# Optimization experiments

Measured on AMD Instinct MI355X. Metric: run time of the kernel, lower is better.

## Reference

```python
import jax, jax.numpy as jnp
import numpy as np

B, S, D, H = 4, 1024, 1024, 16
HD = D // H  # head_dim = 64


def setup_inputs() -> dict:
    key = jax.random.key(0)
    ks = jax.random.split(key, 12)
    inp = {
        "query": jax.random.normal(ks[0], (B, S, D), jnp.float32),
        "key": jax.random.normal(ks[1], (B, S, D), jnp.float32),
        "value": jax.random.normal(ks[2], (B, S, D), jnp.float32),
        # padding mask: 0 = masked, 1 = keep; broadcastable to [B,H,Sq,Sk]
        "mask": jax.random.randint(ks[3], (B, 1, 1, S), 0, 2, jnp.int32),
        # Dense params (Glorot-ish scale)
        "Wq": jax.random.normal(ks[4], (D, D), jnp.float32) / np.sqrt(D),
        "bq": jnp.zeros((D,), jnp.float32),
        "Wk": jax.random.normal(ks[5], (D, D), jnp.float32) / np.sqrt(D),
        "bk": jnp.zeros((D,), jnp.float32),
        "Wv": jax.random.normal(ks[6], (D, D), jnp.float32) / np.sqrt(D),
        "bv": jnp.zeros((D,), jnp.float32),
        "Wo": jax.random.normal(ks[7], (D, D), jnp.float32) / np.sqrt(D),
        "bo": jnp.zeros((D,), jnp.float32),
    }
    return inp


def _split_heads(x):
    # [B, S, D] -> [B, H, S, HD]
    b, s, _ = x.shape
    return x.reshape(b, s, H, HD).transpose(0, 2, 1, 3)


def reference(query, key, value, mask, Wq, bq, Wk, bk, Wv, bv, Wo, bo):
    q = _split_heads(query @ Wq + bq)   # [B,H,S,HD]
    k = _split_heads(key @ Wk + bk)
    v = _split_heads(value @ Wv + bv)

    scale = jnp.sqrt(jnp.asarray(HD, q.dtype))
    energy = jnp.einsum("bhqd,bhkd->bhqk", q, k) / scale  # [B,H,S,S]
    energy = jnp.where(mask == 0, jnp.asarray(-1e10, energy.dtype), energy)
    attention = jax.nn.softmax(energy, axis=-1)
    # dropout is identity at inference
    x = jnp.einsum("bhqk,bhkd->bhqd", attention, v)       # [B,H,S,HD]
    x = x.transpose(0, 2, 1, 3).reshape(query.shape[0], -1, H * HD)  # [B,S,D]
    outputs = x @ Wo + bo
    return outputs, attention
```

## Files before the change

kernel.cpp:

```cpp
#include <hip/hip_runtime.h>

typedef short short8  __attribute__((ext_vector_type(8)));
typedef short short4v __attribute__((ext_vector_type(4)));
typedef float float4v __attribute__((ext_vector_type(4)));
typedef int   int4v   __attribute__((ext_vector_type(4)));

__device__ __forceinline__ short f2bf(float f) {
    unsigned u = __builtin_bit_cast(unsigned, f);
    u += 0x7fff + ((u >> 16) & 1);
    return (short)(u >> 16);
}

__device__ __forceinline__ void gl_lds16(const void* g, void* l) {
    __builtin_amdgcn_global_load_lds(
        (const __attribute__((address_space(1))) void*)g,
        (__attribute__((address_space(3))) void*)l, 16, 0, 0);
}

__global__ __launch_bounds__(256) void prep(
    const float* __restrict__ W0, const float* __restrict__ W1,
    const float* __restrict__ W2, const float* __restrict__ W3,
    short* __restrict__ T0, short* __restrict__ T1,
    short* __restrict__ T2, short* __restrict__ T3,
    const float* __restrict__ qf, const float* __restrict__ kf,
    const float* __restrict__ vf,
    short* __restrict__ Qb, short* __restrict__ Kb, short* __restrict__ Vb)
{
    __shared__ short Tl[64 * 72];
    const int tid = threadIdx.x;
    if (blockIdx.x >= 1024) {
        int cid = blockIdx.x - 1024;
        int arr = cid >> 11;
        const float* src = arr == 0 ? qf : arr == 1 ? kf : vf;
        short*       dst = arr == 0 ? Qb : arr == 1 ? Kb : Vb;
        size_t base = ((size_t)(cid & 2047) * 256 + tid) * 8;
        float4v v0 = *(const float4v*)&src[base];
        float4v v1 = *(const float4v*)&src[base + 4];
        short8 o = {f2bf(v0[0]), f2bf(v0[1]), f2bf(v0[2]), f2bf(v0[3]),
                    f2bf(v1[0]), f2bf(v1[1]), f2bf(v1[2]), f2bf(v1[3])};
        *(short8*)&dst[base] = o;
        return;
    }
    const int mat = blockIdx.x >> 8;
    const int t   = blockIdx.x & 255;
    const int k0 = (t >> 4) * 64, n0 = (t & 15) * 64;
    const float* W = mat == 0 ? W0 : mat == 1 ? W1 : mat == 2 ? W2 : W3;
    short*       T = mat == 0 ? T0 : mat == 1 ? T1 : mat == 2 ? T2 : T3;
    #pragma unroll
    for (int i = 0; i < 4; i++) {
        int c = tid + i * 256;
        int row = c >> 4, c4 = (c & 15) * 4;
        float4v v = *(const float4v*)&W[(size_t)(k0 + row) * 1024 + n0 + c4];
        short4v s = {f2bf(v[0]), f2bf(v[1]), f2bf(v[2]), f2bf(v[3])};
        *(short4v*)&Tl[row * 72 + c4] = s;
    }
    __syncthreads();
    #pragma unroll
    for (int i = 0; i < 2; i++) {
        int c = tid + i * 256;
        int nrow = c >> 3, k8 = (c & 7) * 8;
        short8 v;
        #pragma unroll
        for (int e = 0; e < 8; e++) v[e] = Tl[(k8 + e) * 72 + nrow];
        *(short8*)&T[(size_t)(n0 + nrow) * 1024 + k0 + k8] = v;
    }
}

__device__ __forceinline__ void gemm_body(
    const short* __restrict__ A, const short* __restrict__ Bt,
    short* As, short* Bs, float4v (&acc)[4][2], int m0, int n0, int K)
{
    const int tid = threadIdx.x;
    const int w = tid >> 6, lid = tid & 63, quad = lid >> 4, l15 = lid & 15;
    const int wr = w >> 1, wc = w & 1;
    const int lrow = lid >> 3, lcb = lid & 7;

    for (int kb = 0; kb < K; kb += 64) {
        #pragma unroll
        for (int p = 0; p < 4; p++) {
            int chunk = p * 4 + w;
            int row = chunk * 8 + lrow;
            int cb = lcb ^ (row & 7);
            gl_lds16(&A[(size_t)(m0 + row) * K + kb + cb * 8], &As[chunk * 512]);
        }
        #pragma unroll
        for (int p = 0; p < 2; p++) {
            int chunk = p * 4 + w;
            int row = chunk * 8 + lrow;
            int cb = lcb ^ (row & 7);
            gl_lds16(&Bt[(size_t)(n0 + row) * K + kb + cb * 8], &Bs[chunk * 512]);
        }
        __syncthreads();

        short8 af[4][2], bfr[2][2];
        #pragma unroll
        for (int i = 0; i < 4; i++) {
            int row = wr * 64 + i * 16 + l15;
            int sw = row & 7;
            #pragma unroll
            for (int h = 0; h < 2; h++)
                af[i][h] = *(short8*)&As[row * 64 + ((h * 4 + quad) ^ sw) * 8];
        }
        #pragma unroll
        for (int j = 0; j < 2; j++) {
            int row = wc * 32 + j * 16 + l15;
            int sw = row & 7;
            #pragma unroll
            for (int h = 0; h < 2; h++)
                bfr[j][h] = *(short8*)&Bs[row * 64 + ((h * 4 + quad) ^ sw) * 8];
        }
        #pragma unroll
        for (int i = 0; i < 4; i++)
            #pragma unroll
            for (int j = 0; j < 2; j++) {
                acc[i][j] = __builtin_amdgcn_mfma_f32_16x16x32_bf16(
                    af[i][0], bfr[j][0], acc[i][j], 0, 0, 0);
                acc[i][j] = __builtin_amdgcn_mfma_f32_16x16x32_bf16(
                    af[i][1], bfr[j][1], acc[i][j], 0, 0, 0);
            }
        __syncthreads();
    }
}

__global__ __launch_bounds__(256) void gemm_qkv(
    const short* __restrict__ Ab, const short* __restrict__ Btb,
    const float* __restrict__ b0, const float* __restrict__ b1,
    const float* __restrict__ b2, short* __restrict__ Cq,
    short* __restrict__ Ck, short* __restrict__ Cvt)
{
    __shared__ short As[128 * 64];
    __shared__ short Bs[64 * 64];
    const int zz = blockIdx.z;
    const short* A  = Ab  + (size_t)zz * 4194304;
    const short* Bt = Btb + (size_t)zz * 1048576;
    const float* bias = zz == 0 ? b0 : zz == 1 ? b1 : b2;
    const int m0 = blockIdx.x * 128, n0 = blockIdx.y * 64;

    float4v acc[4][2];
    #pragma unroll
    for (int i = 0; i < 4; i++)
        #pragma unroll
        for (int j = 0; j < 2; j++) acc[i][j] = (float4v){0.f, 0.f, 0.f, 0.f};

    gemm_body(A, Bt, As, Bs, acc, m0, n0, 1024);

    const int tid = threadIdx.x;
    const int w = tid >> 6, lid = tid & 63, quad = lid >> 4, l15 = lid & 15;
    const int wr = w >> 1, wc = w & 1;
    #pragma unroll
    for (int j = 0; j < 2; j++) {
        int n = n0 + wc * 32 + j * 16 + l15;
        float bj = bias[n];
        #pragma unroll
        for (int i = 0; i < 4; i++) {
            if (zz == 2) {
                int b = m0 >> 10;
                int sbase = (m0 & 1023) + wr * 64 + i * 16 + quad * 4;
                short4v sv;
                #pragma unroll
                for (int r = 0; r < 4; r++) sv[r] = f2bf(acc[i][j][r] + bj);
                *(short4v*)&Cvt[(size_t)b * 1048576 + (size_t)n * 1024 + sbase] = sv;
            } else {
                short* C = zz == 0 ? Cq : Ck;
                #pragma unroll
                for (int r = 0; r < 4; r++) {
                    int m = m0 + wr * 64 + i * 16 + quad * 4 + r;
                    C[(size_t)m * 1024 + n] = f2bf(acc[i][j][r] + bj);
                }
            }
        }
    }
}

__global__ __launch_bounds__(256) void gemm_out(
    const short* __restrict__ A, const short* __restrict__ Bt,
    const float* __restrict__ bias, float* __restrict__ C)
{
    __shared__ short As[128 * 64];
    __shared__ short Bs[64 * 64];
    const int m0 = blockIdx.x * 128, n0 = blockIdx.y * 64;
    float4v acc[4][2];
    #pragma unroll
    for (int i = 0; i < 4; i++)
        #pragma unroll
        for (int j = 0; j < 2; j++) acc[i][j] = (float4v){0.f, 0.f, 0.f, 0.f};

    gemm_body(A, Bt, As, Bs, acc, m0, n0, 1024);

    const int tid = threadIdx.x;
    const int w = tid >> 6, lid = tid & 63, quad = lid >> 4, l15 = lid & 15;
    const int wr = w >> 1, wc = w & 1;
    #pragma unroll
    for (int j = 0; j < 2; j++) {
        int n = n0 + wc * 32 + j * 16 + l15;
        float bj = bias[n];
        #pragma unroll
        for (int i = 0; i < 4; i++)
            #pragma unroll
            for (int r = 0; r < 4; r++) {
                int m = m0 + wr * 64 + i * 16 + quad * 4 + r;
                C[(size_t)m * 1024 + n] = acc[i][j][r] + bj;
            }
    }
}

__global__ __launch_bounds__(256, 4) void attn_kernel(
    const short* __restrict__ Qp, const short* __restrict__ Kp,
    const short* __restrict__ Vt, const int* __restrict__ mask,
    float* __restrict__ attnOut, short* __restrict__ X)
{
    __shared__ float SH[4608];
    __shared__ int   maskl[1024];
    __shared__ float redm[4][16];
    __shared__ float redl[4][16];

    const int tid = threadIdx.x;
    const int w = tid >> 6, lid = tid & 63, quad = lid >> 4, l15 = lid & 15;
    const int bid = blockIdx.x;
    const int qb = bid & 63;
    const int bh = bid >> 6;
    const int b = bh >> 4, h = bh & 15;
    const int q0 = qb * 16;
    const size_t rowbase = (size_t)b * 1048576;
    const size_t hoff = (size_t)h * 64;

    *(int4v*)&maskl[tid * 4] = *(const int4v*)&mask[b * 1024 + tid * 4];

    short8 aq0 = *(const short8*)
        &Qp[rowbase + (size_t)(q0 + l15) * 1024 + hoff + quad * 8];
    short8 aq1 = *(const short8*)
        &Qp[rowbase + (size_t)(q0 + l15) * 1024 + hoff + 32 + quad * 8];
    __syncthreads();

    float m_r[4] = {-3e38f, -3e38f, -3e38f, -3e38f};
    float l_r[4] = {0.f, 0.f, 0.f, 0.f};
    #pragma unroll
    for (int nk = 0; nk < 8; nk++) {
        #pragma unroll
        for (int jj = 0; jj < 2; jj++) {
            int n = nk * 128 + w * 32 + jj * 16 + l15;
            const short* kr = &Kp[rowbase + (size_t)n * 1024 + hoff + quad * 8];
            short8 kf0 = *(const short8*)kr;
            short8 kf1 = *(const short8*)(kr + 32);
            float4v acc = (float4v){0.f, 0.f, 0.f, 0.f};
            acc = __builtin_amdgcn_mfma_f32_16x16x32_bf16(aq0, kf0, acc, 0, 0, 0);
            acc = __builtin_amdgcn_mfma_f32_16x16x32_bf16(aq1, kf1, acc, 0, 0, 0);
            bool keep = maskl[n] != 0;
            #pragma unroll
            for (int r = 0; r < 4; r++) {
                float s = keep ? acc[r] * 0.125f : -1e10f;
                float mn = fmaxf(m_r[r], s);
                l_r[r] = l_r[r] * __expf(m_r[r] - mn) + __expf(s - mn);
                m_r[r] = mn;
            }
        }
    }
    #pragma unroll
    for (int off = 1; off < 16; off <<= 1) {
        #pragma unroll
        for (int r = 0; r < 4; r++) {
            float mo = __shfl_xor(m_r[r], off);
            float lo = __shfl_xor(l_r[r], off);
            float mn = fmaxf(m_r[r], mo);
            l_r[r] = l_r[r] * __expf(m_r[r] - mn) + lo * __expf(mo - mn);
            m_r[r] = mn;
        }
    }
    if (l15 == 0) {
        #pragma unroll
        for (int r = 0; r < 4; r++) {
            redm[w][quad * 4 + r] = m_r[r];
            redl[w][quad * 4 + r] = l_r[r];
        }
    }
    __syncthreads();
    float mrow[4], inv[4];
    #pragma unroll
    for (int r = 0; r < 4; r++) {
        int qr = quad * 4 + r;
        float m0 = redm[0][qr], m1 = redm[1][qr];
        float m2 = redm[2][qr], m3 = redm[3][qr];
        float M = fmaxf(fmaxf(m0, m1), fmaxf(m2, m3));
        float L = redl[0][qr] * __expf(m0 - M) + redl[1][qr] * __expf(m1 - M)
                + redl[2][qr] * __expf(m2 - M) + redl[3][qr] * __expf(m3 - M);
        mrow[r] = M;
        inv[r] = 1.0f / L;
    }

    const size_t abase = ((size_t)bh * 1024 + q0) * 1024;
    float* Pw0 = &SH[(size_t)(0 * 4 + w) * 16 * 36];
    float* Pw1 = &SH[(size_t)(1 * 4 + w) * 16 * 36];
    float4v accX[4];
    #pragma unroll
    for (int jj = 0; jj < 4; jj++) accX[jj] = (float4v){0.f, 0.f, 0.f, 0.f};

    #pragma unroll
    for (int kt = 0; kt < 8; kt++) {
        float* Pw = (kt & 1) ? Pw1 : Pw0;
        #pragma unroll
        for (int jj2 = 0; jj2 < 2; jj2++) {
            int n = kt * 128 + w * 32 + jj2 * 16 + l15;
            const short* kr = &Kp[rowbase + (size_t)n * 1024 + hoff + quad * 8];
            short8 kf0 = *(const short8*)kr;
            short8 kf1 = *(const short8*)(kr + 32);
            float4v acc = (float4v){0.f, 0.f, 0.f, 0.f};
            acc = __builtin_amdgcn_mfma_f32_16x16x32_bf16(aq0, kf0, acc, 0, 0, 0);
            acc = __builtin_amdgcn_mfma_f32_16x16x32_bf16(aq1, kf1, acc, 0, 0, 0);
            bool keep = maskl[n] != 0;
            #pragma unroll
            for (int r = 0; r < 4; r++) {
                float s = keep ? acc[r] * 0.125f : -1e10f;
                float p = __expf(s - mrow[r]) * inv[r];
                Pw[(quad * 4 + r) * 36 + jj2 * 16 + l15] = p;
            }
        }
        #pragma unroll
        for (int pass = 0; pass < 2; pass++) {
            int row = pass * 8 + (lid >> 3), c4 = (lid & 7) * 4;
            float4v pv = *(float4v*)&Pw[row * 36 + c4];
            __builtin_nontemporal_store(pv, (float4v*)
                &attnOut[abase + (size_t)row * 1024 + kt * 128 + w * 32 + c4]);
        }
        float4v pa0 = *(float4v*)&Pw[l15 * 36 + quad * 8];
        float4v pa1 = *(float4v*)&Pw[l15 * 36 + quad * 8 + 4];
        short8 ap = {f2bf(pa0[0]), f2bf(pa0[1]), f2bf(pa0[2]), f2bf(pa0[3]),
                     f2bf(pa1[0]), f2bf(pa1[1]), f2bf(pa1[2]), f2bf(pa1[3])};
        #pragma unroll
        for (int jj = 0; jj < 4; jj++) {
            short8 bv = *(const short8*)
                &Vt[rowbase + (hoff + jj * 16 + l15) * 1024 +
                    kt * 128 + w * 32 + quad * 8];
            accX[jj] = __builtin_amdgcn_mfma_f32_16x16x32_bf16(ap, bv, accX[jj], 0, 0, 0);
        }
    }

    __syncthreads();
    float* Xr = SH;
    #pragma unroll
    for (int jj = 0; jj < 4; jj++)
        #pragma unroll
        for (int r = 0; r < 4; r++)
            Xr[(size_t)(w * 16 + quad * 4 + r) * 64 + jj * 16 + l15] = accX[jj][r];
    __syncthreads();
    {
        int q = tid >> 4, d4 = (tid & 15) * 4;
        float4v s0 = *(float4v*)&Xr[(size_t)(0 * 16 + q) * 64 + d4];
        float4v s1 = *(float4v*)&Xr[(size_t)(1 * 16 + q) * 64 + d4];
        float4v s2 = *(float4v*)&Xr[(size_t)(2 * 16 + q) * 64 + d4];
        float4v s3 = *(float4v*)&Xr[(size_t)(3 * 16 + q) * 64 + d4];
        short4v o;
        #pragma unroll
        for (int e = 0; e < 4; e++)
            o[e] = f2bf(s0[e] + s1[e] + s2[e] + s3[e]);
        *(short4v*)&X[rowbase + (size_t)(q0 + q) * 1024 + hoff + d4] = o;
    }
}

extern "C" void kernel_launch(void* const* d_in, const int* in_sizes, int n_in,
                              void* d_out, int out_size, void* d_ws, size_t ws_size,
                              hipStream_t stream)
{
    const float* q_in = (const float*)d_in[0];
    const float* k_in = (const float*)d_in[1];
    const float* v_in = (const float*)d_in[2];
    const int*   mask = (const int*)d_in[3];
    const float* Wq = (const float*)d_in[4];
    const float* bq = (const float*)d_in[5];
    const float* Wk = (const float*)d_in[6];
    const float* bk = (const float*)d_in[7];
    const float* Wv = (const float*)d_in[8];
    const float* bv = (const float*)d_in[9];
    const float* Wo = (const float*)d_in[10];
    const float* bo = (const float*)d_in[11];

    short* ws = (short*)d_ws;
    const size_t MEL = 4096ull * 1024;
    short* Qp  = ws;
    short* Kp  = ws + MEL;
    short* Vt  = ws + 2 * MEL;
    short* Xp  = ws + 3 * MEL;
    short* WqT = ws + 4 * MEL;
    short* WkT = WqT + 1024 * 1024;
    short* WvT = WkT + 1024 * 1024;
    short* WoT = WvT + 1024 * 1024;

    float* outp  = (float*)d_out;
    float* attnp = outp + MEL;

    short* Qb = (short*)attnp;
    short* Kb = Qb + MEL;
    short* Vb = Kb + MEL;

    prep<<<dim3(7168), dim3(256), 0, stream>>>(Wq, Wk, Wv, Wo,
                                               WqT, WkT, WvT, WoT,
                                               q_in, k_in, v_in, Qb, Kb, Vb);
    gemm_qkv<<<dim3(32, 16, 3), 256, 0, stream>>>(Qb, WqT, bq, bk, bv,
                                                  Qp, Kp, Vt);
    attn_kernel<<<dim3(4096), dim3(256), 0, stream>>>(Qp, Kp, Vt, mask, attnp, Xp);
    gemm_out<<<dim3(32, 16), 256, 0, stream>>>(Xp, WoT, bo, outp);
}
```

Measured before the change: 547.6 us.

## Stage K/V tiles in swizzled LDS and give each wave its own query rows

The attention kernel is restructured so each block handles 64 query rows, with each wave owning 16 rows and sweeping all keys. K and V tiles are staged into shared memory via global_load_lds with an XOR swizzle and reused by all four waves, replacing per-wave direct global loads. The softmax stats pass now takes one max per 128-key tile, and the cross-wave reductions and final X reduction through LDS are removed. The block index is remapped to spread heads across XCDs. Grid drops to 1024 blocks with a larger LDS footprint, which may lower occupancy and latency hiding.

```diff
diff --git a/kernel.cpp b/kernel.cpp
--- a/kernel.cpp
+++ b/kernel.cpp
@@ -204,56 +204,96 @@
     }
 }
 
-__global__ __launch_bounds__(256, 4) void attn_kernel(
+__global__ __launch_bounds__(256) void attn_kernel(
     const short* __restrict__ Qp, const short* __restrict__ Kp,
     const short* __restrict__ Vt, const int* __restrict__ mask,
     float* __restrict__ attnOut, short* __restrict__ X)
 {
-    __shared__ float SH[4608];
+    __shared__ short Ks[128 * 64];
+    __shared__ short Vs[64 * 128];
+    __shared__ float Pws[4][16 * 132];
     __shared__ int   maskl[1024];
-    __shared__ float redm[4][16];
-    __shared__ float redl[4][16];
 
     const int tid = threadIdx.x;
     const int w = tid >> 6, lid = tid & 63, quad = lid >> 4, l15 = lid & 15;
-    const int bid = blockIdx.x;
-    const int qb = bid & 63;
-    const int bh = bid >> 6;
+    const int vb = blockIdx.x;
+    const int bid = (vb & 7) * 128 + (vb >> 3);
+    const int qt = bid & 15;
+    const int bh = bid >> 4;
     const int b = bh >> 4, h = bh & 15;
-    const int q0 = qb * 16;
     const size_t rowbase = (size_t)b * 1048576;
     const size_t hoff = (size_t)h * 64;
+    const int q0w = qt * 64 + w * 16;
 
     *(int4v*)&maskl[tid * 4] = *(const int4v*)&mask[b * 1024 + tid * 4];
 
     short8 aq0 = *(const short8*)
-        &Qp[rowbase + (size_t)(q0 + l15) * 1024 + hoff + quad * 8];
+        &Qp[rowbase + (size_t)(q0w + l15) * 1024 + hoff + quad * 8];
     short8 aq1 = *(const short8*)
-        &Qp[rowbase + (size_t)(q0 + l15) * 1024 + hoff + 32 + quad * 8];
-    __syncthreads();
+        &Qp[rowbase + (size_t)(q0w + l15) * 1024 + hoff + 32 + quad * 8];
+
+    const int lrow8 = lid >> 3, lcb8 = lid & 7;
+    const int lrow4 = lid >> 4, lcb16 = lid & 15;
+    auto stageK = [&](short* buf, int kt) {
+        #pragma unroll
+        for (int p = 0; p < 4; p++) {
+            int chunk = p * 4 + w;
+            int row = chunk * 8 + lrow8;
+            int cb = lcb8 ^ (row & 7);
+            gl_lds16(&Kp[rowbase + (size_t)(kt * 128 + row) * 1024 + hoff + cb * 8],
+                     &buf[chunk * 512]);
+        }
+    };
+    auto stageV = [&](short* buf, int kt) {
+        #pragma unroll
+        for (int p = 0; p < 4; p++) {
+            int chunk = p * 4 + w;
+            int row = chunk * 4 + lrow4;
+            int cb = lcb16 ^ (row & 7);
+            gl_lds16(&Vt[rowbase + (size_t)(hoff + row) * 1024 + kt * 128 + cb * 8],
+                     &buf[chunk * 512]);
+        }
+    };
 
     float m_r[4] = {-3e38f, -3e38f, -3e38f, -3e38f};
     float l_r[4] = {0.f, 0.f, 0.f, 0.f};
-    #pragma unroll
-    for (int nk = 0; nk < 8; nk++) {
-        #pragma unroll
-        for (int jj = 0; jj < 2; jj++) {
-            int n = nk * 128 + w * 32 + jj * 16 + l15;
-            const short* kr = &Kp[rowbase + (size_t)n * 1024 + hoff + quad * 8];
-            short8 kf0 = *(const short8*)kr;
-            short8 kf1 = *(const short8*)(kr + 32);
-            float4v acc = (float4v){0.f, 0.f, 0.f, 0.f};
-            acc = __builtin_amdgcn_mfma_f32_16x16x32_bf16(aq0, kf0, acc, 0, 0, 0);
-            acc = __builtin_amdgcn_mfma_f32_16x16x32_bf16(aq1, kf1, acc, 0, 0, 0);
-            bool keep = maskl[n] != 0;
+    stageK(Ks, 0);
+    for (int kt = 0; kt < 8; kt++) {
+        __syncthreads();
+        if (kt + 1 < 8) stageK((kt & 1) ? Ks : Vs, kt + 1);
+        const short* buf = (kt & 1) ? Vs : Ks;
+        float4v accS[8];
+        #pragma unroll
+        for (int jj = 0; jj < 8; jj++) {
+            int row = jj * 16 + l15, sw = row & 7;
+            short8 b0 = *(short8*)&buf[row * 64 + (quad ^ sw) * 8];
+            short8 b1 = *(short8*)&buf[row * 64 + ((4 + quad) ^ sw) * 8];
+            float4v a = (float4v){0.f, 0.f, 0.f, 0.f};
+            a = __builtin_amdgcn_mfma_f32_16x16x32_bf16(aq0, b0, a, 0, 0, 0);
+            accS[jj] = __builtin_amdgcn_mfma_f32_16x16x32_bf16(aq1, b1, a, 0, 0, 0);
+        }
+        float tmax[4] = {-3e38f, -3e38f, -3e38f, -3e38f};
+        #pragma unroll
+        for (int jj = 0; jj < 8; jj++) {
+            bool keep = maskl[kt * 128 + jj * 16 + l15] != 0;
             #pragma unroll
             for (int r = 0; r < 4; r++) {
-                float s = keep ? acc[r] * 0.125f : -1e10f;
-                float mn = fmaxf(m_r[r], s);
-                l_r[r] = l_r[r] * __expf(m_r[r] - mn) + __expf(s - mn);
-                m_r[r] = mn;
-            }
-        }
+                float s = keep ? accS[jj][r] * 0.125f : -1e10f;
+                accS[jj][r] = s;
+                tmax[r] = fmaxf(tmax[r], s);
+            }
+        }
+        #pragma unroll
+        for (int r = 0; r < 4; r++) {
+            float mn = fmaxf(m_r[r], tmax[r]);
+            l_r[r] *= __expf(m_r[r] - mn);
+            m_r[r] = mn;
+        }
+        #pragma unroll
+        for (int jj = 0; jj < 8; jj++)
+            #pragma unroll
+            for (int r = 0; r < 4; r++)
+                l_r[r] += __expf(accS[jj][r] - m_r[r]);
     }
     #pragma unroll
     for (int off = 1; off < 16; off <<= 1) {
@@ -266,94 +306,67 @@
             m_r[r] = mn;
         }
     }
-    if (l15 == 0) {
-        #pragma unroll
-        for (int r = 0; r < 4; r++) {
-            redm[w][quad * 4 + r] = m_r[r];
-            redl[w][quad * 4 + r] = l_r[r];
-        }
-    }
-    __syncthreads();
-    float mrow[4], inv[4];
-    #pragma unroll
-    for (int r = 0; r < 4; r++) {
-        int qr = quad * 4 + r;
-        float m0 = redm[0][qr], m1 = redm[1][qr];
-        float m2 = redm[2][qr], m3 = redm[3][qr];
-        float M = fmaxf(fmaxf(m0, m1), fmaxf(m2, m3));
-        float L = redl[0][qr] * __expf(m0 - M) + redl[1][qr] * __expf(m1 - M)
-                + redl[2][qr] * __expf(m2 - M) + redl[3][qr] * __expf(m3 - M);
-        mrow[r] = M;
-        inv[r] = 1.0f / L;
-    }
-
-    const size_t abase = ((size_t)bh * 1024 + q0) * 1024;
-    float* Pw0 = &SH[(size_t)(0 * 4 + w) * 16 * 36];
-    float* Pw1 = &SH[(size_t)(1 * 4 + w) * 16 * 36];
+    float inv[4];
+    #pragma unroll
+    for (int r = 0; r < 4; r++) inv[r] = 1.0f / l_r[r];
+
+    const size_t abase = ((size_t)bh * 1024 + q0w) * 1024;
+    float* Pw = &Pws[w][0];
     float4v accX[4];
     #pragma unroll
-    for (int jj = 0; jj < 4; jj++) accX[jj] = (float4v){0.f, 0.f, 0.f, 0.f};
-
-    #pragma unroll
+    for (int jd = 0; jd < 4; jd++) accX[jd] = (float4v){0.f, 0.f, 0.f, 0.f};
+
     for (int kt = 0; kt < 8; kt++) {
-        float* Pw = (kt & 1) ? Pw1 : Pw0;
-        #pragma unroll
-        for (int jj2 = 0; jj2 < 2; jj2++) {
-            int n = kt * 128 + w * 32 + jj2 * 16 + l15;
-            const short* kr = &Kp[rowbase + (size_t)n * 1024 + hoff + quad * 8];
-            short8 kf0 = *(const short8*)kr;
-            short8 kf1 = *(const short8*)(kr + 32);
-            float4v acc = (float4v){0.f, 0.f, 0.f, 0.f};
-            acc = __builtin_amdgcn_mfma_f32_16x16x32_bf16(aq0, kf0, acc, 0, 0, 0);
-            acc = __builtin_amdgcn_mfma_f32_16x16x32_bf16(aq1, kf1, acc, 0, 0, 0);
-            bool keep = maskl[n] != 0;
+        __syncthreads();
+        stageK(Ks, kt);
+        stageV(Vs, kt);
+        __syncthreads();
+        #pragma unroll
+        for (int jj = 0; jj < 8; jj++) {
+            int row = jj * 16 + l15, sw = row & 7;
+            short8 b0 = *(short8*)&Ks[row * 64 + (quad ^ sw) * 8];
+            short8 b1 = *(short8*)&Ks[row * 64 + ((4 + quad) ^ sw) * 8];
+            float4v a = (float4v){0.f, 0.f, 0.f, 0.f};
+            a = __builtin_amdgcn_mfma_f32_16x16x32_bf16(aq0, b0, a, 0, 0, 0);
+            a = __builtin_amdgcn_mfma_f32_16x16x32_bf16(aq1, b1, a, 0, 0, 0);
+            bool keep = maskl[kt * 128 + jj * 16 + l15] != 0;
             #pragma unroll
             for (int r = 0; r < 4; r++) {
-                float s = keep ? acc[r] * 0.125f : -1e10f;
-                float p = __expf(s - mrow[r]) * inv[r];
-                Pw[(quad * 4 + r) * 36 + jj2 * 16 + l15] = p;
-            }
-        }
-        #pragma unroll
-        for (int pass = 0; pass < 2; pass++) {
-            int row = pass * 8 + (lid >> 3), c4 = (lid & 7) * 4;
-            float4v pv = *(float4v*)&Pw[row * 36 + c4];
+                float s = keep ? a[r] * 0.125f : -1e10f;
+                Pw[(quad * 4 + r) * 132 + jj * 16 + l15] =
+                    __expf(s - m_r[r]) * inv[r];
+            }
+        }
+        #pragma unroll
+        for (int pass = 0; pass < 8; pass++) {
+            int row = pass * 2 + (lid >> 5), c4 = (lid & 31) * 4;
+            float4v pv = *(float4v*)&Pw[row * 132 + c4];
             __builtin_nontemporal_store(pv, (float4v*)
-                &attnOut[abase + (size_t)row * 1024 + kt * 128 + w * 32 + c4]);
-        }
-        float4v pa0 = *(float4v*)&Pw[l15 * 36 + quad * 8];
-        float4v pa1 = *(float4v*)&Pw[l15 * 36 + quad * 8 + 4];
-        short8 ap = {f2bf(pa0[0]), f2bf(pa0[1]), f2bf(pa0[2]), f2bf(pa0[3]),
-                     f2bf(pa1[0]), f2bf(pa1[1]), f2bf(pa1[2]), f2bf(pa1[3])};
-        #pragma unroll
-        for (int jj = 0; jj < 4; jj++) {
-            short8 bv = *(const short8*)
-                &Vt[rowbase + (hoff + jj * 16 + l15) * 1024 +
-                    kt * 128 + w * 32 + quad * 8];
-            accX[jj] = __builtin_amdgcn_mfma_f32_16x16x32_bf16(ap, bv, accX[jj], 0, 0, 0);
-        }
-    }
-
-    __syncthreads();
-    float* Xr = SH;
-    #pragma unroll
-    for (int jj = 0; jj < 4; jj++)
+                &attnOut[abase + (size_t)row * 1024 + kt * 128 + c4]);
+        }
+        #pragma unroll
+        for (int ks = 0; ks < 4; ks++) {
+            float4v pa0 = *(float4v*)&Pw[l15 * 132 + ks * 32 + quad * 8];
+            float4v pa1 = *(float4v*)&Pw[l15 * 132 + ks * 32 + quad * 8 + 4];
+            short8 ap = {f2bf(pa0[0]), f2bf(pa0[1]), f2bf(pa0[2]), f2bf(pa0[3]),
+                         f2bf(pa1[0]), f2bf(pa1[1]), f2bf(pa1[2]), f2bf(pa1[3])};
+            #pragma unroll
+            for (int jd = 0; jd < 4; jd++) {
+                int vrow = jd * 16 + l15;
+                int cbv = (ks * 4 + quad) ^ (vrow & 7);
+                short8 bv = *(short8*)&Vs[vrow * 128 + cbv * 8];
+                accX[jd] = __builtin_amdgcn_mfma_f32_16x16x32_bf16(
+                    ap, bv, accX[jd], 0, 0, 0);
+            }
+        }
+    }
+
+    #pragma unroll
+    for (int jd = 0; jd < 4; jd++)
         #pragma unroll
         for (int r = 0; r < 4; r++)
-            Xr[(size_t)(w * 16 + quad * 4 + r) * 64 + jj * 16 + l15] = accX[jj][r];
-    __syncthreads();
-    {
-        int q = tid >> 4, d4 = (tid & 15) * 4;
-        float4v s0 = *(float4v*)&Xr[(size_t)(0 * 16 + q) * 64 + d4];
-        float4v s1 = *(float4v*)&Xr[(size_t)(1 * 16 + q) * 64 + d4];
-        float4v s2 = *(float4v*)&Xr[(size_t)(2 * 16 + q) * 64 + d4];
-        float4v s3 = *(float4v*)&Xr[(size_t)(3 * 16 + q) * 64 + d4];
-        short4v o;
-        #pragma unroll
-        for (int e = 0; e < 4; e++)
-            o[e] = f2bf(s0[e] + s1[e] + s2[e] + s3[e]);
-        *(short4v*)&X[rowbase + (size_t)(q0 + q) * 1024 + hoff + d4] = o;
-    }
+            X[rowbase + (size_t)(q0w + quad * 4 + r) * 1024 + hoff + jd * 16 + l15] =
+                f2bf(accX[jd][r]);
 }
 
 extern "C" void kernel_launch(void* const* d_in, const int* in_sizes, int n_in,
@@ -396,6 +409,6 @@
                                                q_in, k_in, v_in, Qb, Kb, Vb);
     gemm_qkv<<<dim3(32, 16, 3), 256, 0, stream>>>(Qb, WqT, bq, bk, bv,
                                                   Qp, Kp, Vt);
-    attn_kernel<<<dim3(4096), dim3(256), 0, stream>>>(Qp, Kp, Vt, mask, attnp, Xp);
+    attn_kernel<<<dim3(1024), dim3(256), 0, stream>>>(Qp, Kp, Vt, mask, attnp, Xp);
     gemm_out<<<dim3(32, 16), 256, 0, stream>>>(Xp, WoT, bo, outp);
 }
```

Result: faster. 445.4 us (-18.7%).
